# Kernel tuning notes

Hardware: AMD Instinct MI355X
Metric: run time of the kernel (lower is better)

## Reference

```python
import jax, jax.numpy as jnp
import numpy as np

V = 4096          # total nodes (pedestrian + group)
F = 64            # input feature dim
H = 16            # hidden dim
CTX = 4           # context (phi) dim
P = 3072          # num_ped_nodes
G = 1024          # group conflict matrix size
EPS = 1e-8
SLOPE = 0.2


def setup_inputs() -> dict:
    key = jax.random.key(0)
    ks = jax.random.split(key, 8)
    node_features = jax.random.normal(ks[0], (V, F), dtype=jnp.float32)
    a = jax.random.uniform(ks[1], (V, V), dtype=jnp.float32)
    adjacency = jnp.where(a > 0.9, a, 0.0)
    node_positions = jax.random.normal(ks[2], (V, 2), dtype=jnp.float32) * 10.0
    node_velocities = jax.random.normal(ks[3], (V, 2), dtype=jnp.float32)
    node_types = jax.random.randint(ks[4], (V,), 0, 2, dtype=jnp.int64)
    conflict_softmax_group = jax.random.uniform(ks[5], (G, G), dtype=jnp.float32)
    W_proj = jax.random.normal(ks[6], (F, H), dtype=jnp.float32) * 0.1
    w_score = jax.random.normal(ks[7], (2 * H + CTX,), dtype=jnp.float32) * 0.1
    return {
        "node_features": node_features,
        "adjacency": adjacency,
        "node_positions": node_positions,
        "node_velocities": node_velocities,
        "node_types": node_types,
        "num_ped_nodes": P,
        "conflict_softmax_group": conflict_softmax_group,
        "W_proj": W_proj,
        "w_score": w_score,
    }


def reference(node_features, adjacency, node_positions, node_velocities,
              node_types, num_ped_nodes, conflict_softmax_group, W_proj, w_score):
    v = node_features.shape[0]
    hdim = W_proj.shape[1]

    h = node_features @ W_proj  # [V, H]

    # --- phi = [dist, vel_diff, dir_align, norm_conf] : [V, V, 4] ---
    dpos = node_positions[:, None, :] - node_positions[None, :, :]   # [V,V,2]
    dist = jnp.linalg.norm(dpos, axis=-1)                            # [V,V]
    dvel = node_velocities[:, None, :] - node_velocities[None, :, :]
    vel_diff = jnp.linalg.norm(dvel, axis=-1)
    speed = jnp.linalg.norm(node_velocities, axis=-1, keepdims=True)
    dirv = node_velocities / (speed + EPS)                           # [V,2]
    dir_align = jnp.clip(dirv @ dirv.T, -1.0, 1.0)                   # [V,V]

    # vectorized replacement of the Python double-loop scatter:
    g = jnp.arange(v) - num_ped_nodes
    gsize = conflict_softmax_group.shape[0]
    valid = (node_types == 1) & (g >= 0) & (g < gsize)               # [V]
    gc = jnp.clip(g, 0, gsize - 1)
    norm_conf = jnp.where(valid[:, None] & valid[None, :],
                          conflict_softmax_group[gc[:, None], gc[None, :]], 0.0)

    phi = jnp.stack([dist, vel_diff, dir_align, norm_conf], axis=-1)  # [V,V,4]

    # --- attention score: concat([h_i, h_j, phi]) @ w_score, decomposed to
    # avoid materializing the [V,V,2H+4] pair tensor (same math) ---
    li = h @ w_score[:hdim]             # [V]  contribution of h_i
    lj = h @ w_score[hdim:2 * hdim]     # [V]  contribution of h_j
    logits = li[:, None] + lj[None, :] + phi @ w_score[2 * hdim:]    # [V,V]
    logits = jnp.where(logits >= 0, logits, SLOPE * logits)          # LeakyReLU

    suppress = jnp.where(adjacency > 0, 0.0, -1e9)
    attn = jax.nn.softmax(logits + suppress, axis=1)
    attn = attn * adjacency
    attn = attn / (attn.sum(axis=1, keepdims=True) + EPS)
    attended = attn @ h                 # [V, H]
    return attended, attn, phi
```

## Files before the change

### kernel.cpp

```cpp
#include <hip/hip_runtime.h>

#define V 4096
#define F 64
#define H 16
#define GSZ 1024
#define EPS 1e-8f
#define SLOPE 0.2f
#define NITER (V / 256)

typedef float f4 __attribute__((ext_vector_type(4)));
typedef unsigned int u32;

__device__ __forceinline__ u32 pack_bf16(float x, float y) {
    u32 bx = __float_as_uint(x);
    u32 by = __float_as_uint(y);
    bx += 0x7fffu + ((bx >> 16) & 1u);
    by += 0x7fffu + ((by >> 16) & 1u);
    return (bx >> 16) | (by & 0xffff0000u);
}

__global__ __launch_bounds__(256) void prep_kernel(
    const float* __restrict__ feat,
    const float* __restrict__ pos,
    const float* __restrict__ vel,
    const int*   __restrict__ types,
    const int*   __restrict__ nped,
    const float* __restrict__ Wp,
    const float* __restrict__ wscore,
    uint4* __restrict__ hgA,
    uint4* __restrict__ hgB,
    float* __restrict__ li,
    f4*    __restrict__ na,
    f4*    __restrict__ nb)
{
    int i = blockIdx.x * blockDim.x + threadIdx.x;
    if (i >= V) return;

    float acc[H];
#pragma unroll
    for (int c = 0; c < H; ++c) acc[c] = 0.f;
    for (int f = 0; f < F; ++f) {
        float x = feat[i * F + f];
#pragma unroll
        for (int c = 0; c < H; ++c) acc[c] += x * Wp[f * H + c];
    }
    float sli = 0.f, slj = 0.f;
#pragma unroll
    for (int c = 0; c < H; ++c) {
        sli += acc[c] * wscore[c];
        slj += acc[c] * wscore[H + c];
    }
    uint4 wa, wb;
    wa.x = pack_bf16(acc[0], acc[1]);   wa.y = pack_bf16(acc[2], acc[3]);
    wa.z = pack_bf16(acc[4], acc[5]);   wa.w = pack_bf16(acc[6], acc[7]);
    wb.x = pack_bf16(acc[8], acc[9]);   wb.y = pack_bf16(acc[10], acc[11]);
    wb.z = pack_bf16(acc[12], acc[13]); wb.w = pack_bf16(acc[14], acc[15]);
    hgA[i] = wa;
    hgB[i] = wb;
    li[i] = sli;

    float vx = vel[i * 2], vy = vel[i * 2 + 1];
    float inv = 1.f / (sqrtf(vx * vx + vy * vy) + EPS);
    int P = nped[0];
    int g = i - P;
    int gc = (types[i] == 1 && g >= 0 && g < GSZ) ? g : -1;

    f4 A, B;
    A.x = pos[i * 2]; A.y = pos[i * 2 + 1]; A.z = vx; A.w = vy;
    B.x = vx * inv;   B.y = vy * inv;       B.z = slj; B.w = __int_as_float(gc);
    na[i] = A;
    nb[i] = B;
}

__global__ __launch_bounds__(256) void row_kernel(
    const float* __restrict__ adj,
    const float* __restrict__ conflict,
    const float* __restrict__ wscore,
    const uint4* __restrict__ hgA,
    const uint4* __restrict__ hgB,
    const float* __restrict__ li,
    const f4*    __restrict__ na,
    const f4*    __restrict__ nb,
    float* __restrict__ out_att,
    float* __restrict__ out_attn,
    float* __restrict__ out_phi)
{
    const int i   = blockIdx.x;
    const int tid = threadIdx.x;

    __shared__ float ea_lds[V];
    __shared__ float red[4];
    __shared__ float atile[4 * H];

    const f4 ra = na[i];
    const f4 rb = nb[i];
    const float pix = ra.x, piy = ra.y, vix = ra.z, viy = ra.w;
    const float dix = rb.x, diy = rb.y;
    const int   gi  = __float_as_int(rb.w);
    const float li_i = li[i];
    const float w0 = wscore[2 * H + 0];
    const float w1 = wscore[2 * H + 1];
    const float w2 = wscore[2 * H + 2];
    const float w3 = wscore[2 * H + 3];

    const float* adjrow  = adj + (size_t)i * V;
    f4*          phirow  = (f4*)out_phi + (size_t)i * V;
    float*       attnrow = out_attn + (size_t)i * V;

    float acch[8];
#pragma unroll
    for (int c = 0; c < 8; ++c) acch[c] = 0.f;
    float t = 0.f;
#pragma unroll 4
    for (int k = 0; k < NITER; ++k) {
        int j = tid + k * 256;
        float a = adjrow[j];
        f4 A = na[j];
        f4 B = nb[j];
        float dx = pix - A.x, dy = piy - A.y;
        float dist = sqrtf(dx * dx + dy * dy);
        float dvx = vix - A.z, dvy = viy - A.w;
        float vdiff = sqrtf(dvx * dvx + dvy * dvy);
        float al = fminf(1.f, fmaxf(-1.f, dix * B.x + diy * B.y));
        int gj = __float_as_int(B.w);
        float conf = (gi >= 0 && gj >= 0) ? conflict[(size_t)gi * GSZ + gj] : 0.f;

        f4 ph;
        ph.x = dist; ph.y = vdiff; ph.z = al; ph.w = conf;
        __builtin_nontemporal_store(ph, phirow + j);

        float lg = li_i + B.z + dist * w0 + vdiff * w1 + al * w2 + conf * w3;
        lg = (lg >= 0.f) ? lg : SLOPE * lg;
        float e = (a > 0.f) ? __expf(fminf(lg, 80.f)) : 0.f;
        float eav = e * a;
        ea_lds[k * 256 + tid] = eav;
        t += eav;

        uint4 wb = hgB[j];
        acch[0] += eav * __uint_as_float(wb.x << 16);
        acch[1] += eav * __uint_as_float(wb.x & 0xffff0000u);
        acch[2] += eav * __uint_as_float(wb.y << 16);
        acch[3] += eav * __uint_as_float(wb.y & 0xffff0000u);
        acch[4] += eav * __uint_as_float(wb.z << 16);
        acch[5] += eav * __uint_as_float(wb.z & 0xffff0000u);
        acch[6] += eav * __uint_as_float(wb.w << 16);
        acch[7] += eav * __uint_as_float(wb.w & 0xffff0000u);
    }
#pragma unroll
    for (int off = 32; off; off >>= 1) t += __shfl_xor(t, off);
    if ((tid & 63) == 0) red[tid >> 6] = t;
    __syncthreads();
    t = red[0] + red[1] + red[2] + red[3];
    const float dinv = (t > 0.f) ? 1.f / t : 0.f;

    {
        float acc[8];
#pragma unroll
        for (int c = 0; c < 8; ++c) acc[c] = 0.f;
#pragma unroll 4
        for (int k = 0; k < NITER; ++k) {
            int j = tid + k * 256;
            float w = ea_lds[k * 256 + tid] * dinv;
            __builtin_nontemporal_store(w, attnrow + j);
            uint4 wa = hgA[j];
            acc[0] += w * __uint_as_float(wa.x << 16);
            acc[1] += w * __uint_as_float(wa.x & 0xffff0000u);
            acc[2] += w * __uint_as_float(wa.y << 16);
            acc[3] += w * __uint_as_float(wa.y & 0xffff0000u);
            acc[4] += w * __uint_as_float(wa.z << 16);
            acc[5] += w * __uint_as_float(wa.z & 0xffff0000u);
            acc[6] += w * __uint_as_float(wa.w << 16);
            acc[7] += w * __uint_as_float(wa.w & 0xffff0000u);
        }
#pragma unroll
        for (int c = 0; c < 8; ++c)
#pragma unroll
            for (int off = 32; off; off >>= 1) acc[c] += __shfl_xor(acc[c], off);
        if ((tid & 63) == 0) {
            int wv = tid >> 6;
#pragma unroll
            for (int c = 0; c < 8; ++c) atile[wv * H + c] = acc[c];
        }
    }

#pragma unroll
    for (int c = 0; c < 8; ++c)
#pragma unroll
        for (int off = 32; off; off >>= 1) acch[c] += __shfl_xor(acch[c], off);
    if ((tid & 63) == 0) {
        int wv = tid >> 6;
#pragma unroll
        for (int c = 0; c < 8; ++c) atile[wv * H + 8 + c] = acch[c] * dinv;
    }

    __syncthreads();
    if (tid < H) {
        out_att[(size_t)i * H + tid] =
            atile[tid] + atile[H + tid] + atile[2 * H + tid] + atile[3 * H + tid];
    }
}

extern "C" void kernel_launch(void* const* d_in, const int* in_sizes, int n_in,
                              void* d_out, int out_size, void* d_ws, size_t ws_size,
                              hipStream_t stream) {
    const float* feat     = (const float*)d_in[0];
    const float* adj      = (const float*)d_in[1];
    const float* pos      = (const float*)d_in[2];
    const float* vel      = (const float*)d_in[3];
    const int*   types    = (const int*)  d_in[4];
    const int*   nped     = (const int*)  d_in[5];
    const float* conflict = (const float*)d_in[6];
    const float* Wp       = (const float*)d_in[7];
    const float* wscore   = (const float*)d_in[8];

    float* out = (float*)d_out;
    float* out_att  = out;
    float* out_attn = out + (size_t)V * H;
    float* out_phi  = out + (size_t)V * H + (size_t)V * V;

    float* ws = (float*)d_ws;
    uint4* hgA = (uint4*)ws;
    uint4* hgB = hgA + V;
    float* li  = (float*)(hgB + V);
    f4*    na  = (f4*)(li + V);
    f4*    nb  = na + V;

    prep_kernel<<<dim3(V / 256), dim3(256), 0, stream>>>(
        feat, pos, vel, types, nped, Wp, wscore, hgA, hgB, li, na, nb);

    row_kernel<<<dim3(V), dim3(256), 0, stream>>>(
        adj, conflict, wscore, hgA, hgB, li, na, nb, out_att, out_attn, out_phi);
}
```

Measured before the change: 86.16 us.

## Split phi output writing into a separate kernel from the row attention kernel

Moves the 256 MB phi tensor store out of the fused row kernel into a dedicated phi_kernel launched before it. The row kernel still recomputes phi features for the logits but no longer writes them. This unfuses the work, so the phi features are computed twice and there is an extra launch. The likely intent is to ease pressure on the row kernel's store path or registers, at the cost of the duplicated compute.

```diff
diff --git a/kernel.cpp b/kernel.cpp
--- a/kernel.cpp
+++ b/kernel.cpp
@@ -72,6 +72,41 @@
     nb[i] = B;
 }
 
+__global__ __launch_bounds__(256) void phi_kernel(
+    const float* __restrict__ conflict,
+    const f4*    __restrict__ na,
+    const f4*    __restrict__ nb,
+    float* __restrict__ out_phi)
+{
+    const int bid = blockIdx.x;
+    const int i   = bid >> 2;
+    const int jb  = (bid & 3) * 1024;
+    const int tid = threadIdx.x;
+
+    const f4 ra = na[i];
+    const f4 rb = nb[i];
+    const int gi = __float_as_int(rb.w);
+
+    f4* phirow = (f4*)out_phi + (size_t)i * V + jb;
+
+#pragma unroll
+    for (int k = 0; k < 4; ++k) {
+        int j = jb + tid + k * 256;
+        f4 A = na[j];
+        f4 B = nb[j];
+        float dx = ra.x - A.x, dy = ra.y - A.y;
+        float dist = sqrtf(dx * dx + dy * dy);
+        float dvx = ra.z - A.z, dvy = ra.w - A.w;
+        float vdiff = sqrtf(dvx * dvx + dvy * dvy);
+        float al = fminf(1.f, fmaxf(-1.f, rb.x * B.x + rb.y * B.y));
+        int gj = __float_as_int(B.w);
+        float conf = (gi >= 0 && gj >= 0) ? conflict[(size_t)gi * GSZ + gj] : 0.f;
+        f4 ph;
+        ph.x = dist; ph.y = vdiff; ph.z = al; ph.w = conf;
+        __builtin_nontemporal_store(ph, phirow + tid + k * 256);
+    }
+}
+
 __global__ __launch_bounds__(256) void row_kernel(
     const float* __restrict__ adj,
     const float* __restrict__ conflict,
@@ -82,8 +117,7 @@
     const f4*    __restrict__ na,
     const f4*    __restrict__ nb,
     float* __restrict__ out_att,
-    float* __restrict__ out_attn,
-    float* __restrict__ out_phi)
+    float* __restrict__ out_attn)
 {
     const int i   = blockIdx.x;
     const int tid = threadIdx.x;
@@ -104,7 +138,6 @@
     const float w3 = wscore[2 * H + 3];
 
     const float* adjrow  = adj + (size_t)i * V;
-    f4*          phirow  = (f4*)out_phi + (size_t)i * V;
     float*       attnrow = out_attn + (size_t)i * V;
 
     float acch[8];
@@ -124,10 +157,6 @@
         float al = fminf(1.f, fmaxf(-1.f, dix * B.x + diy * B.y));
         int gj = __float_as_int(B.w);
         float conf = (gi >= 0 && gj >= 0) ? conflict[(size_t)gi * GSZ + gj] : 0.f;
-
-        f4 ph;
-        ph.x = dist; ph.y = vdiff; ph.z = al; ph.w = conf;
-        __builtin_nontemporal_store(ph, phirow + j);
 
         float lg = li_i + B.z + dist * w0 + vdiff * w1 + al * w2 + conf * w3;
         lg = (lg >= 0.f) ? lg : SLOPE * lg;
@@ -228,6 +257,9 @@
     prep_kernel<<<dim3(V / 256), dim3(256), 0, stream>>>(
         feat, pos, vel, types, nped, Wp, wscore, hgA, hgB, li, na, nb);
 
+    phi_kernel<<<dim3(V * 4), dim3(256), 0, stream>>>(
+        conflict, na, nb, out_phi);
+
     row_kernel<<<dim3(V), dim3(256), 0, stream>>>(
-        adj, conflict, wscore, hgA, hgB, li, na, nb, out_att, out_attn, out_phi);
-}
+        adj, conflict, wscore, hgA, hgB, li, na, nb, out_att, out_attn);
+}
```

Measured after the change: 117.2 us. 1.36x slower.
